# Kernel optimization log

Measured on AMD Instinct MI355X. Metric: run time of the kernel, lower is better.

Reference implementation:

```python
import jax, jax.numpy as jnp
import numpy as np

B, N, D, K = 64, 512, 256, 1024
LIMIT = float(np.sqrt(K))   # default initialize_limit = num_embeddings ** 0.5
BN_EPS = 1e-5               # torch BatchNorm1d default eps


def setup_inputs() -> dict:
    key = jax.random.key(0)
    k1, k2, k3 = jax.random.split(key, 3)
    x = jax.random.normal(k1, (B, N, D), jnp.float32)
    atom_mask = jax.random.randint(k2, (B, N), 0, 2, jnp.int32)
    e_i_ts = jax.random.uniform(k3, (D, K), jnp.float32, -LIMIT, LIMIT)
    return {
        "x": x,
        "atom_mask": atom_mask,
        "e_i_ts": e_i_ts,
        "bn_gamma": jnp.ones((D,), jnp.float32),
        "bn_beta": jnp.zeros((D,), jnp.float32),
    }


def reference(x, atom_mask, e_i_ts, bn_gamma, bn_beta):
    flat = x.reshape(-1, D)                          # [BN, D]
    m = atom_mask.reshape(-1).astype(flat.dtype)     # [BN], 1 = valid atom
    n_valid = jnp.maximum(m.sum(), 1.0)

    # BatchNorm1d (training mode) over valid atoms only (torch applies BN to
    # the gathered rows). Biased variance, as in torch's normalization.
    mu = (m[:, None] * flat).sum(0) / n_valid
    var = (m[:, None] * (flat - mu) ** 2).sum(0) / n_valid
    xb = (flat - mu) * jax.lax.rsqrt(var + BN_EPS) * bn_gamma + bn_beta

    # squared-distance to codebook + argmin + gather
    d = (xb ** 2).sum(1, keepdims=True) - 2.0 * (xb @ e_i_ts) + (e_i_ts ** 2).sum(0, keepdims=True)  # [BN, K]
    idx = jnp.argmin(d, axis=1)                      # [BN]
    q = e_i_ts.T[idx]                                # [BN, D] quantized (valid-row semantics)

    # scatter back into padded tensor (padded rows -> 0), straight-through
    q_pad = (m[:, None] * q).reshape(x.shape)
    quantized_x = x + jax.lax.stop_gradient(q_pad - x)

    sg = jax.lax.stop_gradient
    dictionary_loss = (m[:, None] * (sg(xb) - q) ** 2).sum() / (n_valid * D)
    commitment_loss = (m[:, None] * (xb - sg(q)) ** 2).sum() / (n_valid * D)

    # perplexity over valid atoms
    counts = jnp.zeros((K,), flat.dtype).at[idx].add(m)
    avg_probs = counts / n_valid
    perplexity = jnp.exp(-jnp.sum(avg_probs * jnp.log(avg_probs + 1e-10)))

    idx_out = jnp.where(m > 0, idx, -1)[:, None]     # [BN, 1]; -1 marks padded rows
    return quantized_x, dictionary_loss, commitment_loss, idx_out, perplexity
```

## Files before the change

### kernel.cpp

```cpp
#include <hip/hip_runtime.h>
#include <math.h>

#define BN   32768
#define DIM  256
#define KC   1024
#define BN_EPS 1e-5f

#define QX_SIZE   (BN * DIM)
#define LOSS0_OFF (QX_SIZE)
#define LOSS1_OFF (QX_SIZE + 1)
#define IDX_OFF   (QX_SIZE + 2)
#define PERP_OFF  (QX_SIZE + 2 + BN)

#define PART_V 0
#define PART_I (NSLICE * BN)

#define WS_SUM    0
#define WS_SUMSQ  256
#define WS_COUNT  512
#define WS_LOSS   513
#define WS_COUNTS 1024
#define WS_CNORM  3072
#define WS_PK     8192
#define WS_ETX    (8192 + 262144)
#define WS_MINKEY (8192 + 262144 + 262144)
#define WS_ET_LEG 8192

#define NSLICE 4
#define SLICEK (KC / NSLICE)
#define NGRP   (SLICEK / 64)

typedef short bf16x8  __attribute__((ext_vector_type(8)));
typedef float f32x4   __attribute__((ext_vector_type(4)));
typedef float fvec4   __attribute__((ext_vector_type(4)));
typedef int   int4v   __attribute__((ext_vector_type(4)));
typedef unsigned long long u64;

static __device__ inline unsigned short f2bf(float f) {
    unsigned int u = __float_as_uint(f);
    return (unsigned short)((u + 0x7FFFu + ((u >> 16) & 1u)) >> 16);
}
static __device__ inline fvec4 nt_ld4(const void* p) {
    return __builtin_nontemporal_load((const fvec4*)p);
}
static __device__ inline void nt_st(float* p, float v) {
    __builtin_nontemporal_store(v, p);
}
static __device__ inline unsigned enc_f32(float f) {
    unsigned u = __float_as_uint(f);
    return (u & 0x80000000u) ? ~u : (u | 0x80000000u);
}

__global__ __launch_bounds__(256) void k_pre(const float* __restrict__ x,
                                             const int* __restrict__ mask,
                                             const float* __restrict__ e,
                                             float* __restrict__ ws,
                                             int use_et, int use_pk, int et_off) {
    int t = threadIdx.x;
    int b = blockIdx.x;
    if (b >= 260) {
        if (!use_et && !use_pk) return;
        int b2 = b - 260;
        int d0 = (b2 >> 4) * 64;
        int k0 = (b2 & 15) * 64;
        __shared__ float tile[64][65];
        int c = t & 63;
        int rq = t >> 6;
        #pragma unroll
        for (int p = 0; p < 16; ++p) {
            int dd = p * 4 + rq;
            tile[dd][c] = e[(size_t)(d0 + dd) * KC + k0 + c];
        }
        __syncthreads();
        if (use_et) {
            #pragma unroll
            for (int p = 0; p < 16; ++p) {
                int kk = p * 4 + rq;
                nt_st(&ws[et_off + (size_t)(k0 + kk) * DIM + d0 + c],
                      tile[c][kk]);
            }
        }
        if (use_pk) {
            char* pk = (char*)(ws + WS_PK);
            int lane2 = t & 63;
            int fgrp = t >> 6;
            int quad2 = lane2 >> 4, col2 = lane2 & 15;
            int G = b2 & 15;
            #pragma unroll
            for (int p = 0; p < 4; ++p) {
                int fi = fgrp * 4 + p;
                int kcl = fi >> 3;
                int nt = (fi >> 1) & 3;
                int h = fi & 1;
                int kcg = (b2 >> 4) * 2 + kcl;
                bf16x8 ov;
                #pragma unroll
                for (int j = 0; j < 8; ++j) {
                    float v = tile[kcl * 32 + quad2 * 8 + j][nt * 16 + col2];
                    unsigned u = __float_as_uint(v);
                    if (h == 0) {
                        ov[j] = (short)(u >> 16);
                    } else {
                        float lf = v - __uint_as_float(u & 0xffff0000u);
                        ov[j] = (short)(__float_as_uint(lf) >> 16);
                    }
                }
                size_t off = ((size_t)((G * 8 + kcg) * 8 + nt * 2 + h) << 10)
                             + (size_t)lane2 * 16;
                *(bf16x8*)(pk + off) = ov;
            }
        }
        return;
    }
    if (b >= 256) {
        int k = (b - 256) * 256 + t;
        float acc = 0.f;
        #pragma unroll 8
        for (int d = 0; d < DIM; ++d) {
            float v = e[(size_t)d * KC + k];
            acc = fmaf(v, v, acc);
        }
        ws[WS_CNORM + k] = acc;
        return;
    }
    __shared__ float s4[4 * 256];
    __shared__ float q4[4 * 256];
    __shared__ float cntS[4];
    int c4 = t & 63;
    int rsub = t >> 6;
    float s0=0.f,s1=0.f,s2=0.f,s3=0.f, q0=0.f,q1=0.f,q2=0.f,q3=0.f, cnt=0.f;
    int rbase = b * 4 + rsub;
    for (int i = 0; i < 32; ++i) {
        int r = rbase + i * 1024;
        float m = (float)mask[r];
        fvec4 v = nt_ld4(&x[(size_t)r * DIM + c4 * 4]);
        cnt += m;
        float m0 = m*v.x, m1 = m*v.y, m2 = m*v.z, m3 = m*v.w;
        s0 += m0; s1 += m1; s2 += m2; s3 += m3;
        q0 = fmaf(m0, v.x, q0); q1 = fmaf(m1, v.y, q1);
        q2 = fmaf(m2, v.z, q2); q3 = fmaf(m3, v.w, q3);
    }
    int f = c4 * 4;
    s4[rsub * 256 + f + 0] = s0; s4[rsub * 256 + f + 1] = s1;
    s4[rsub * 256 + f + 2] = s2; s4[rsub * 256 + f + 3] = s3;
    q4[rsub * 256 + f + 0] = q0; q4[rsub * 256 + f + 1] = q1;
    q4[rsub * 256 + f + 2] = q2; q4[rsub * 256 + f + 3] = q3;
    if (c4 == 0) cntS[rsub] = cnt;
    __syncthreads();
    float stot = s4[t] + s4[256 + t] + s4[512 + t] + s4[768 + t];
    float qtot = q4[t] + q4[256 + t] + q4[512 + t] + q4[768 + t];
    atomicAdd(&ws[WS_SUM + t], stot);
    atomicAdd(&ws[WS_SUMSQ + t], qtot);
    if (t == 0)
        atomicAdd(&ws[WS_COUNT], cntS[0] + cntS[1] + cntS[2] + cntS[3]);
}

__global__ __launch_bounds__(512) void k_packA(
        const float* __restrict__ x, const float* __restrict__ gamma,
        const float* __restrict__ beta, const float* __restrict__ ws,
        float* __restrict__ out) {
    __shared__ float muS[DIM], scS[DIM], btS[DIM];
    const int tid = threadIdx.x;
    const int row0 = blockIdx.x * 128;
    const int w = tid >> 6;
    const int lane = tid & 63;
    const int quad = lane >> 4;
    const int col0 = lane & 15;
    if (tid < 256) {
        float cnt = ws[WS_COUNT];
        float nv = fmaxf(cnt, 1.f);
        float mu = ws[WS_SUM + tid] / nv;
        float var = ws[WS_SUMSQ + tid] / nv - mu * mu;
        var = fmaxf(var, 0.f);
        muS[tid] = mu;
        scS[tid] = rsqrtf(var + BN_EPS) * gamma[tid];
        btS[tid] = beta[tid];
    }
    __syncthreads();
    const float* xr = x + (size_t)(row0 + w * 16 + col0) * DIM;
    char* pa = (char*)out + (size_t)(blockIdx.x * 8 + w) * 16384;
    #pragma unroll
    for (int kc = 0; kc < 8; ++kc) {
        int k0 = kc * 32 + quad * 8;
        fvec4 v0 = nt_ld4(xr + k0);
        fvec4 v1 = nt_ld4(xr + k0 + 4);
        float xv[8] = {v0.x, v0.y, v0.z, v0.w, v1.x, v1.y, v1.z, v1.w};
        bf16x8 hv, lv;
        #pragma unroll
        for (int j = 0; j < 8; ++j) {
            float xb = fmaf(xv[j] - muS[k0 + j], scS[k0 + j], btS[k0 + j]);
            unsigned short h = f2bf(xb);
            float hf = __uint_as_float((unsigned)h << 16);
            hv[j] = (short)h;
            lv[j] = (short)f2bf(xb - hf);
        }
        __builtin_nontemporal_store(hv,
            (bf16x8*)(pa + (kc * 2 + 0) * 1024 + lane * 16));
        __builtin_nontemporal_store(lv,
            (bf16x8*)(pa + (kc * 2 + 1) * 1024 + lane * 16));
    }
}


#define CHUNK_COMPUTE(slot, kcc)                                             \
    {                                                                        \
        const char* bufb = &Bs[(slot) * 8192];                               \
        __builtin_amdgcn_s_setprio(1);                                       \
        _Pragma("unroll")                                                    \
        for (int nt = 0; nt < 4; ++nt) {                                     \
            bf16x8 bh = *(const bf16x8*)(bufb + (nt * 2 + 0) * 1024 + lane * 16); \
            bf16x8 bl = *(const bf16x8*)(bufb + (nt * 2 + 1) * 1024 + lane * 16); \
            acc[nt] = __builtin_amdgcn_mfma_f32_16x16x32_bf16(ah[kcc], bh, acc[nt], 0, 0, 0); \
            acc[nt] = __builtin_amdgcn_mfma_f32_16x16x32_bf16(ah[kcc], bl, acc[nt], 0, 0, 0); \
            acc[nt] = __builtin_amdgcn_mfma_f32_16x16x32_bf16(al[kcc], bh, acc[nt], 0, 0, 0); \
        }                                                                    \
        __builtin_amdgcn_s_setprio(0);                                       \
    }

#define SCORE_MERGE(gg)                                                      \
    {                                                                        \
        _Pragma("unroll")                                                    \
        for (int r = 0; r < 4; ++r) {                                        \
            float v = 3.4e38f; int ii = 0;                                   \
            _Pragma("unroll")                                                \
            for (int nt = 0; nt < 4; ++nt) {                                 \
                int kl = (gg) * 64 + nt * 16 + col0;                         \
                float sc = fmaf(-2.f, acc[nt][r], cnS[kl]);                  \
                if (sc < v) { v = sc; ii = kl; }                             \
            }                                                                \
            _Pragma("unroll")                                                \
            for (int m2 = 1; m2 < 16; m2 <<= 1) {                            \
                float v2 = __shfl_xor(v, m2, 64);                            \
                int   i2 = __shfl_xor(ii, m2, 64);                           \
                if (v2 < v || (v2 == v && i2 < ii)) { v = v2; ii = i2; }     \
            }                                                                \
            if (v < bv[r] || (v == bv[r] && ii < bi_[r])) {                  \
                bv[r] = v; bi_[r] = ii;                                      \
            }                                                                \
        }                                                                    \
        _Pragma("unroll")                                                    \
        for (int nt = 0; nt < 4; ++nt)                                       \
            acc[nt] = (f32x4){0.f, 0.f, 0.f, 0.f};                           \
    }

__global__ __launch_bounds__(512, 4) void k_main_mfma(
        const float* __restrict__ x, const int* __restrict__ mask,
        const float* __restrict__ e, const float* __restrict__ gamma,
        const float* __restrict__ beta,
        float* __restrict__ ws, float* __restrict__ out,
        int use_pk, int use_mk, int use_pa) {
    __shared__ __align__(16) char Bs[4 * 8192];
    __shared__ float muS[DIM], scS[DIM], btS[DIM];
    __shared__ float cnS[SLICEK];

    const int tid = threadIdx.x;
    const int rb = blockIdx.x >> 2;
    const int s = blockIdx.x & 3;
    const int row0 = rb * 128;
    const int w = tid >> 6;
    const int lane = tid & 63;
    const int quad = lane >> 4;
    const int col0 = lane & 15;

    if (!use_pa && tid < 256) {
        float cnt = ws[WS_COUNT];
        float nv = fmaxf(cnt, 1.f);
        float mu = ws[WS_SUM + tid] / nv;
        float var = ws[WS_SUMSQ + tid] / nv - mu * mu;
        var = fmaxf(var, 0.f);
        muS[tid] = mu;
        scS[tid] = rsqrtf(var + BN_EPS) * gamma[tid];
        btS[tid] = beta[tid];
    }
    if (tid < SLICEK)
        cnS[tid] = ws[WS_CNORM + s * SLICEK + tid];
    __syncthreads();

    bf16x8 ah[8], al[8];
    if (use_pa) {
        const char* pa = (const char*)out + (size_t)(rb * 8 + w) * 16384;
        #pragma unroll
        for (int kc = 0; kc < 8; ++kc) {
            ah[kc] = *(const bf16x8*)(pa + (kc * 2 + 0) * 1024 + lane * 16);
            al[kc] = *(const bf16x8*)(pa + (kc * 2 + 1) * 1024 + lane * 16);
        }
    } else {
        const float* xr = x + (size_t)(row0 + w * 16 + col0) * DIM;
        #pragma unroll
        for (int kc = 0; kc < 8; ++kc) {
            int k0 = kc * 32 + quad * 8;
            fvec4 v0 = nt_ld4(xr + k0);
            fvec4 v1 = nt_ld4(xr + k0 + 4);
            float xv[8] = {v0.x, v0.y, v0.z, v0.w, v1.x, v1.y, v1.z, v1.w};
            bf16x8 hv, lv;
            #pragma unroll
            for (int j = 0; j < 8; ++j) {
                float xb = fmaf(xv[j] - muS[k0 + j], scS[k0 + j], btS[k0 + j]);
                unsigned short h = f2bf(xb);
                float hf = __uint_as_float((unsigned)h << 16);
                hv[j] = (short)h;
                lv[j] = (short)f2bf(xb - hf);
            }
            ah[kc] = hv;
            al[kc] = lv;
        }
    }
    asm volatile("s_waitcnt vmcnt(0)" ::: "memory");
    __builtin_amdgcn_sched_barrier(0);

    f32x4 acc[4];
    #pragma unroll
    for (int nt = 0; nt < 4; ++nt)
        acc[nt] = (f32x4){0.f, 0.f, 0.f, 0.f};
    float bv[4] = {3.4e38f, 3.4e38f, 3.4e38f, 3.4e38f};
    int   bi_[4] = {0, 0, 0, 0};

    if (use_pk) {
        const char* pkb = (const char*)(ws + WS_PK)
                          + (size_t)s * (NGRP * 8 * 8192);
        auto stage = [&](int c2, int slot) {
            const char* src = pkb + (size_t)c2 * 8192 + w * 1024 + lane * 16;
            char* dst = &Bs[slot * 8192 + w * 1024];
            __builtin_amdgcn_global_load_lds(
                (const __attribute__((address_space(1))) void*)src,
                (__attribute__((address_space(3))) void*)dst, 16, 0, 0);
        };
        stage(0, 0);
        stage(1, 1);
        for (int g = 0; g < NGRP - 1; ++g) {
            #pragma unroll
            for (int kc = 0; kc < 8; ++kc) {
                stage(g * 8 + kc + 2, (kc + 2) & 3);
                asm volatile("s_waitcnt vmcnt(2)" ::: "memory");
                __builtin_amdgcn_s_barrier();
                __builtin_amdgcn_sched_barrier(0);
                CHUNK_COMPUTE(kc & 3, kc);
            }
            SCORE_MERGE(g);
        }
        {
            #pragma unroll
            for (int kc = 0; kc < 8; ++kc) {
                if (kc < 6) {
                    stage((NGRP - 1) * 8 + kc + 2, (kc + 2) & 3);
                    asm volatile("s_waitcnt vmcnt(2)" ::: "memory");
                } else if (kc == 6) {
                    asm volatile("s_waitcnt vmcnt(1)" ::: "memory");
                } else {
                    asm volatile("s_waitcnt vmcnt(0)" ::: "memory");
                }
                __builtin_amdgcn_s_barrier();
                __builtin_amdgcn_sched_barrier(0);
                CHUNK_COMPUTE(kc & 3, kc);
            }
            SCORE_MERGE(NGRP - 1);
        }
    } else {
        for (int g = 0; g < NGRP; ++g) {
            #pragma unroll
            for (int kc = 0; kc < 8; ++kc) {
                const float* ep = e + (size_t)(kc * 32 + quad * 8) * KC
                                    + s * SLICEK + g * 64 + col0;
                #pragma unroll
                for (int nt = 0; nt < 4; ++nt) {
                    const float* epn = ep + nt * 16;
                    float bvv[8];
                    #pragma unroll
                    for (int j = 0; j < 8; ++j)
                        bvv[j] = epn[(size_t)j * KC];
                    int4v hw, lw;
                    #pragma unroll
                    for (int p = 0; p < 4; ++p) {
                        unsigned u0 = __float_as_uint(bvv[2 * p]);
                        unsigned u1 = __float_as_uint(bvv[2 * p + 1]);
                        hw[p] = (int)__builtin_amdgcn_perm(u1, u0, 0x07060302u);
                        float l0 = bvv[2 * p]     - __uint_as_float(u0 & 0xffff0000u);
                        float l1 = bvv[2 * p + 1] - __uint_as_float(u1 & 0xffff0000u);
                        lw[p] = (int)__builtin_amdgcn_perm(__float_as_uint(l1),
                                                           __float_as_uint(l0),
                                                           0x07060302u);
                    }
                    bf16x8 bh = __builtin_bit_cast(bf16x8, hw);
                    bf16x8 bl = __builtin_bit_cast(bf16x8, lw);
                    acc[nt] = __builtin_amdgcn_mfma_f32_16x16x32_bf16(ah[kc], bh, acc[nt], 0, 0, 0);
                    acc[nt] = __builtin_amdgcn_mfma_f32_16x16x32_bf16(ah[kc], bl, acc[nt], 0, 0, 0);
                    acc[nt] = __builtin_amdgcn_mfma_f32_16x16x32_bf16(al[kc], bh, acc[nt], 0, 0, 0);
                }
            }
            SCORE_MERGE(g);
        }
    }

    if (col0 == 0) {
        if (use_mk) {
            u64* mk = (u64*)(ws + WS_MINKEY);
            #pragma unroll
            for (int r = 0; r < 4; ++r) {
                int rl = w * 16 + quad * 4 + r;
                u64 key = ((u64)enc_f32(bv[r]) << 32)
                          | (unsigned)(s * SLICEK + bi_[r]);
                atomicMin(&mk[row0 + rl], key);
            }
        } else {
            #pragma unroll
            for (int r = 0; r < 4; ++r) {
                int rl = w * 16 + quad * 4 + r;
                out[PART_V + s * BN + row0 + rl] = bv[r];
                out[PART_I + s * BN + row0 + rl] = (float)(s * SLICEK + bi_[r]);
            }
        }
    }
}

__global__ __launch_bounds__(256) void k_merge(const int* __restrict__ mask,
                                               float* __restrict__ ws,
                                               float* __restrict__ out) {
    int row = blockIdx.x * 256 + threadIdx.x;
    float bvv = out[PART_V + row];
    int bii = (int)out[PART_I + row];
    #pragma unroll
    for (int s = 1; s < NSLICE; ++s) {
        float v = out[PART_V + s * BN + row];
        int i = (int)out[PART_I + s * BN + row];
        if (v < bvv || (v == bvv && i < bii)) { bvv = v; bii = i; }
    }
    int m = mask[row];
    out[IDX_OFF + row] = m ? (float)bii : -1.0f;
    if (m) atomicAdd(&ws[WS_COUNTS + bii], 1.0f);
}

__global__ __launch_bounds__(256) void k_epi(
        const float* __restrict__ x, const int* __restrict__ mask,
        const float* __restrict__ e, const float* __restrict__ gamma,
        const float* __restrict__ beta,
        const float* __restrict__ ws, float* __restrict__ out,
        int use_et, int et_off, int use_mk) {
    __shared__ __align__(16) float muS[DIM], scS[DIM], btS[DIM];
    __shared__ int   histC[KC];
    __shared__ float wred[4];
    const int tid = threadIdx.x;
    const int row0 = blockIdx.x * 32;
    const int w = tid >> 6;
    const int lane = tid & 63;
    {
        float cnt = ws[WS_COUNT];
        float nv = fmaxf(cnt, 1.f);
        float mu = ws[WS_SUM + tid] / nv;
        float var = ws[WS_SUMSQ + tid] / nv - mu * mu;
        var = fmaxf(var, 0.f);
        muS[tid] = mu;
        scS[tid] = rsqrtf(var + BN_EPS) * gamma[tid];
        btS[tid] = beta[tid];
    }
    #pragma unroll
    for (int j = 0; j < KC / 256; ++j)
        histC[j * 256 + tid] = 0;
    __syncthreads();

    u64 mykey = 0; int mym = 0;
    if (use_mk && lane < 8) {
        const u64* mk = (const u64*)(ws + WS_MINKEY);
        mykey = mk[row0 + w * 8 + lane];
        mym = mask[row0 + w * 8 + lane];
    }

    const int d0 = lane * 4;
    fvec4 mu4 = *(const fvec4*)&muS[d0];
    fvec4 sc4 = *(const fvec4*)&scS[d0];
    fvec4 bt4 = *(const fvec4*)&btS[d0];
    const float* et = ws + et_off;
    float lacc = 0.f;
    int pidx = -1;
    fvec4 g = (fvec4){0.f, 0.f, 0.f, 0.f};
    #pragma unroll
    for (int rr = 0; rr < 8; ++rr) {
        const int row = row0 + w * 8 + rr;
        int m, idx;
        if (use_mk) {
            u64 k = __shfl(mykey, rr, 64);
            m = __shfl(mym, rr, 64);
            idx = (int)(unsigned)(k & 0xFFFFFFFFull);
            if (lane == 0) {
                out[IDX_OFF + row] = m ? (float)idx : -1.0f;
                if (m) atomicAdd(&histC[idx], 1);
            }
        } else {
            m = mask[row];
            idx = m ? (int)out[IDX_OFF + row] : 0;
        }
        const float fm = (float)m;
        fvec4 xv = nt_ld4(&x[(size_t)row * DIM + d0]);
        if (idx != pidx) {
            if (use_mk || !use_et) {
                g.x = e[(size_t)(d0 + 0) * KC + idx];
                g.y = e[(size_t)(d0 + 1) * KC + idx];
                g.z = e[(size_t)(d0 + 2) * KC + idx];
                g.w = e[(size_t)(d0 + 3) * KC + idx];
            } else {
                g = nt_ld4(&et[(size_t)idx * DIM + d0]);
            }
            pidx = idx;
        }
        fvec4 q;
        float dsum = 0.f;
        #pragma unroll
        for (int i = 0; i < 4; ++i) {
            float xb = fmaf(xv[i] - mu4[i], sc4[i], bt4[i]);
            float diff = xb - g[i];
            dsum = fmaf(diff, diff, dsum);
            q[i] = fm * g[i];
        }
        lacc = fmaf(fm, dsum, lacc);
        __builtin_nontemporal_store(q, (fvec4*)&out[(size_t)row * DIM + d0]);
    }
    #pragma unroll
    for (int off2 = 32; off2 > 0; off2 >>= 1)
        lacc += __shfl_down(lacc, off2, 64);
    if (lane == 0) wred[w] = lacc;
    __syncthreads();
    if (use_mk) {
        #pragma unroll
        for (int j = 0; j < KC / 256; ++j) {
            int c = histC[j * 256 + tid];
            if (c > 0) atomicAdd((float*)&ws[WS_COUNTS + j * 256 + tid],
                                 (float)c);
        }
    }
    if (tid == 0)
        atomicAdd((float*)&ws[WS_LOSS], wred[0] + wred[1] + wred[2] + wred[3]);
}

__global__ __launch_bounds__(256) void k_final(const float* __restrict__ ws,
                                               float* __restrict__ out) {
    int t = threadIdx.x;
    __shared__ float wr[4];
    float nv = fmaxf(ws[WS_COUNT], 1.f);
    float acc = 0.f;
    for (int j = t; j < KC; j += 256) {
        float p = ws[WS_COUNTS + j] / nv;
        acc = fmaf(p, logf(p + 1e-10f), acc);
    }
    #pragma unroll
    for (int off = 32; off > 0; off >>= 1) acc += __shfl_down(acc, off, 64);
    if ((t & 63) == 0) wr[t >> 6] = acc;
    __syncthreads();
    if (t == 0) {
        float ent = wr[0] + wr[1] + wr[2] + wr[3];
        float loss = ws[WS_LOSS] / (nv * (float)DIM);
        out[LOSS0_OFF] = loss;
        out[LOSS1_OFF] = loss;
        out[PERP_OFF] = expf(-ent);
    }
}

extern "C" void kernel_launch(void* const* d_in, const int* in_sizes, int n_in,
                              void* d_out, int out_size, void* d_ws, size_t ws_size,
                              hipStream_t stream) {
    const float* x     = (const float*)d_in[0];
    const int*   amask = (const int*)d_in[1];
    const float* e     = (const float*)d_in[2];
    const float* gamma = (const float*)d_in[3];
    const float* beta  = (const float*)d_in[4];
    float* out = (float*)d_out;
    float* ws  = (float*)d_ws;

    size_t need_mk = (size_t)(WS_MINKEY + 2 * BN) * sizeof(float);
    size_t need_pk = (size_t)(WS_ETX + KC * DIM) * sizeof(float);
    size_t need_et = (size_t)(WS_ET_LEG + KC * DIM) * sizeof(float);
    int use_pk = ws_size >= need_pk;
    int use_mk = use_pk && (ws_size >= need_mk);
    int use_pa = use_pk && use_mk;
    int use_et = use_mk ? 0 : (use_pk ? 1 : (ws_size >= need_et ? 1 : 0));
    int et_off = use_pk ? WS_ETX : WS_ET_LEG;

    (void)hipMemsetAsync(d_ws, 0, 32768, stream);
    if (use_mk)
        (void)hipMemsetAsync((char*)d_ws + (size_t)WS_MINKEY * 4, 0xFF,
                             (size_t)BN * 8, stream);

    k_pre<<<324, 256, 0, stream>>>(x, amask, e, ws, use_et, use_pk, et_off);
    if (use_pa)
        k_packA<<<BN / 128, 512, 0, stream>>>(x, gamma, beta, ws, out);
    k_main_mfma<<<256 * NSLICE, 512, 0, stream>>>(x, amask, e, gamma, beta, ws,
                                                  out, use_pk, use_mk, use_pa);
    if (!use_mk)
        k_merge<<<BN / 256, 256, 0, stream>>>(amask, ws, out);
    k_epi<<<BN / 32, 256, 0, stream>>>(x, amask, e, gamma, beta, ws, out,
                                       use_et, et_off, use_mk);
    k_final<<<1, 256, 0, stream>>>(ws, out);
}
```

Before: 229.5 us.

## Retile MFMA waves to 2x2 row-by-codeword tiles with cross-wave argmin merge

```diff
diff --git a/kernel.cpp b/kernel.cpp
--- a/kernel.cpp
+++ b/kernel.cpp
@@ -207,12 +207,19 @@
         const char* bufb = &Bs[(slot) * 8192];                               \
         __builtin_amdgcn_s_setprio(1);                                       \
         _Pragma("unroll")                                                    \
-        for (int nt = 0; nt < 4; ++nt) {                                     \
-            bf16x8 bh = *(const bf16x8*)(bufb + (nt * 2 + 0) * 1024 + lane * 16); \
-            bf16x8 bl = *(const bf16x8*)(bufb + (nt * 2 + 1) * 1024 + lane * 16); \
-            acc[nt] = __builtin_amdgcn_mfma_f32_16x16x32_bf16(ah[kcc], bh, acc[nt], 0, 0, 0); \
-            acc[nt] = __builtin_amdgcn_mfma_f32_16x16x32_bf16(ah[kcc], bl, acc[nt], 0, 0, 0); \
-            acc[nt] = __builtin_amdgcn_mfma_f32_16x16x32_bf16(al[kcc], bh, acc[nt], 0, 0, 0); \
+        for (int nt = 0; nt < 2; ++nt) {                                     \
+            const int ntg = ch * 2 + nt;                                     \
+            bf16x8 bh = *(const bf16x8*)(bufb + (ntg * 2 + 0) * 1024 + lane * 16); \
+            bf16x8 bl = *(const bf16x8*)(bufb + (ntg * 2 + 1) * 1024 + lane * 16); \
+            _Pragma("unroll")                                                \
+            for (int mt = 0; mt < 2; ++mt) {                                 \
+                acc[mt][nt] = __builtin_amdgcn_mfma_f32_16x16x32_bf16(       \
+                    ah[mt][kcc], bh, acc[mt][nt], 0, 0, 0);                  \
+                acc[mt][nt] = __builtin_amdgcn_mfma_f32_16x16x32_bf16(       \
+                    ah[mt][kcc], bl, acc[mt][nt], 0, 0, 0);                  \
+                acc[mt][nt] = __builtin_amdgcn_mfma_f32_16x16x32_bf16(       \
+                    al[mt][kcc], bh, acc[mt][nt], 0, 0, 0);                  \
+            }                                                                \
         }                                                                    \
         __builtin_amdgcn_s_setprio(0);                                       \
     }
@@ -220,30 +227,31 @@
 #define SCORE_MERGE(gg)                                                      \
     {                                                                        \
         _Pragma("unroll")                                                    \
-        for (int r = 0; r < 4; ++r) {                                        \
-            float v = 3.4e38f; int ii = 0;                                   \
+        for (int mt = 0; mt < 2; ++mt) {                                     \
             _Pragma("unroll")                                                \
-            for (int nt = 0; nt < 4; ++nt) {                                 \
-                int kl = (gg) * 64 + nt * 16 + col0;                         \
-                float sc = fmaf(-2.f, acc[nt][r], cnS[kl]);                  \
-                if (sc < v) { v = sc; ii = kl; }                             \
-            }                                                                \
-            _Pragma("unroll")                                                \
-            for (int m2 = 1; m2 < 16; m2 <<= 1) {                            \
-                float v2 = __shfl_xor(v, m2, 64);                            \
-                int   i2 = __shfl_xor(ii, m2, 64);                           \
-                if (v2 < v || (v2 == v && i2 < ii)) { v = v2; ii = i2; }     \
-            }                                                                \
-            if (v < bv[r] || (v == bv[r] && ii < bi_[r])) {                  \
-                bv[r] = v; bi_[r] = ii;                                      \
+            for (int r = 0; r < 4; ++r) {                                    \
+                float v = 3.4e38f; int ii = 0;                               \
+                _Pragma("unroll")                                            \
+                for (int nt = 0; nt < 2; ++nt) {                             \
+                    int kl = (gg) * 64 + (ch * 2 + nt) * 16 + col0;          \
+                    float sc = fmaf(-2.f, acc[mt][nt][r], cnS[kl]);          \
+                    if (sc < v) { v = sc; ii = kl; }                         \
+                    acc[mt][nt][r] = 0.f;                                    \
+                }                                                            \
+                _Pragma("unroll")                                            \
+                for (int m2 = 1; m2 < 16; m2 <<= 1) {                        \
+                    float v2 = __shfl_xor(v, m2, 64);                        \
+                    int   i2 = __shfl_xor(ii, m2, 64);                       \
+                    if (v2 < v || (v2 == v && i2 < ii)) { v = v2; ii = i2; } \
+                }                                                            \
+                if (v < bv[mt][r] || (v == bv[mt][r] && ii < bi_[mt][r])) {  \
+                    bv[mt][r] = v; bi_[mt][r] = ii;                          \
+                }                                                            \
             }                                                                \
         }                                                                    \
-        _Pragma("unroll")                                                    \
-        for (int nt = 0; nt < 4; ++nt)                                       \
-            acc[nt] = (f32x4){0.f, 0.f, 0.f, 0.f};                           \
-    }
-
-__global__ __launch_bounds__(512, 4) void k_main_mfma(
+    }
+
+__global__ __launch_bounds__(512, 2) void k_main_mfma(
         const float* __restrict__ x, const int* __restrict__ mask,
         const float* __restrict__ e, const float* __restrict__ gamma,
         const float* __restrict__ beta,
@@ -252,12 +260,16 @@
     __shared__ __align__(16) char Bs[4 * 8192];
     __shared__ float muS[DIM], scS[DIM], btS[DIM];
     __shared__ float cnS[SLICEK];
+    __shared__ float fvS[128];
+    __shared__ int   fiS[128];
 
     const int tid = threadIdx.x;
     const int rb = blockIdx.x >> 2;
     const int s = blockIdx.x & 3;
     const int row0 = rb * 128;
     const int w = tid >> 6;
+    const int rg = w >> 1;
+    const int ch = w & 1;
     const int lane = tid & 63;
     const int quad = lane >> 4;
     const int col0 = lane & 15;
@@ -276,44 +288,57 @@
         cnS[tid] = ws[WS_CNORM + s * SLICEK + tid];
     __syncthreads();
 
-    bf16x8 ah[8], al[8];
+    bf16x8 ah[2][8], al[2][8];
     if (use_pa) {
-        const char* pa = (const char*)out + (size_t)(rb * 8 + w) * 16384;
-        #pragma unroll
-        for (int kc = 0; kc < 8; ++kc) {
-            ah[kc] = *(const bf16x8*)(pa + (kc * 2 + 0) * 1024 + lane * 16);
-            al[kc] = *(const bf16x8*)(pa + (kc * 2 + 1) * 1024 + lane * 16);
-        }
+        const char* pa = (const char*)out + (size_t)(rb * 8 + rg * 2) * 16384;
+        #pragma unroll
+        for (int mt = 0; mt < 2; ++mt)
+            #pragma unroll
+            for (int kc = 0; kc < 8; ++kc) {
+                ah[mt][kc] = *(const bf16x8*)(pa + mt * 16384
+                                              + (kc * 2 + 0) * 1024 + lane * 16);
+                al[mt][kc] = *(const bf16x8*)(pa + mt * 16384
+                                              + (kc * 2 + 1) * 1024 + lane * 16);
+            }
     } else {
-        const float* xr = x + (size_t)(row0 + w * 16 + col0) * DIM;
-        #pragma unroll
-        for (int kc = 0; kc < 8; ++kc) {
-            int k0 = kc * 32 + quad * 8;
-            fvec4 v0 = nt_ld4(xr + k0);
-            fvec4 v1 = nt_ld4(xr + k0 + 4);
-            float xv[8] = {v0.x, v0.y, v0.z, v0.w, v1.x, v1.y, v1.z, v1.w};
-            bf16x8 hv, lv;
-            #pragma unroll
-            for (int j = 0; j < 8; ++j) {
-                float xb = fmaf(xv[j] - muS[k0 + j], scS[k0 + j], btS[k0 + j]);
-                unsigned short h = f2bf(xb);
-                float hf = __uint_as_float((unsigned)h << 16);
-                hv[j] = (short)h;
-                lv[j] = (short)f2bf(xb - hf);
-            }
-            ah[kc] = hv;
-            al[kc] = lv;
+        #pragma unroll
+        for (int mt = 0; mt < 2; ++mt) {
+            const float* xr = x + (size_t)(row0 + (rg * 2 + mt) * 16 + col0) * DIM;
+            #pragma unroll
+            for (int kc = 0; kc < 8; ++kc) {
+                int k0 = kc * 32 + quad * 8;
+                fvec4 v0 = nt_ld4(xr + k0);
+                fvec4 v1 = nt_ld4(xr + k0 + 4);
+                float xv[8] = {v0.x, v0.y, v0.z, v0.w, v1.x, v1.y, v1.z, v1.w};
+                bf16x8 hv, lv;
+                #pragma unroll
+                for (int j = 0; j < 8; ++j) {
+                    float xb = fmaf(xv[j] - muS[k0 + j], scS[k0 + j], btS[k0 + j]);
+                    unsigned short h = f2bf(xb);
+                    float hf = __uint_as_float((unsigned)h << 16);
+                    hv[j] = (short)h;
+                    lv[j] = (short)f2bf(xb - hf);
+                }
+                ah[mt][kc] = hv;
+                al[mt][kc] = lv;
+            }
         }
     }
     asm volatile("s_waitcnt vmcnt(0)" ::: "memory");
     __builtin_amdgcn_sched_barrier(0);
 
-    f32x4 acc[4];
-    #pragma unroll
-    for (int nt = 0; nt < 4; ++nt)
-        acc[nt] = (f32x4){0.f, 0.f, 0.f, 0.f};
-    float bv[4] = {3.4e38f, 3.4e38f, 3.4e38f, 3.4e38f};
-    int   bi_[4] = {0, 0, 0, 0};
+    f32x4 acc[2][2];
+    #pragma unroll
+    for (int mt = 0; mt < 2; ++mt)
+        #pragma unroll
+        for (int nt = 0; nt < 2; ++nt)
+            acc[mt][nt] = (f32x4){0.f, 0.f, 0.f, 0.f};
+    float bv[2][4];
+    int   bi_[2][4];
+    #pragma unroll
+    for (int mt = 0; mt < 2; ++mt)
+        #pragma unroll
+        for (int r = 0; r < 4; ++r) { bv[mt][r] = 3.4e38f; bi_[mt][r] = 0; }
 
     if (use_pk) {
         const char* pkb = (const char*)(ws + WS_PK)
@@ -362,8 +387,8 @@
                 const float* ep = e + (size_t)(kc * 32 + quad * 8) * KC
                                     + s * SLICEK + g * 64 + col0;
                 #pragma unroll
-                for (int nt = 0; nt < 4; ++nt) {
-                    const float* epn = ep + nt * 16;
+                for (int nt = 0; nt < 2; ++nt) {
+                    const float* epn = ep + (ch * 2 + nt) * 16;
                     float bvv[8];
                     #pragma unroll
                     for (int j = 0; j < 8; ++j)
@@ -382,32 +407,58 @@
                     }
                     bf16x8 bh = __builtin_bit_cast(bf16x8, hw);
                     bf16x8 bl = __builtin_bit_cast(bf16x8, lw);
-                    acc[nt] = __builtin_amdgcn_mfma_f32_16x16x32_bf16(ah[kc], bh, acc[nt], 0, 0, 0);
-                    acc[nt] = __builtin_amdgcn_mfma_f32_16x16x32_bf16(ah[kc], bl, acc[nt], 0, 0, 0);
-                    acc[nt] = __builtin_amdgcn_mfma_f32_16x16x32_bf16(al[kc], bh, acc[nt], 0, 0, 0);
+                    #pragma unroll
+                    for (int mt = 0; mt < 2; ++mt) {
+                        acc[mt][nt] = __builtin_amdgcn_mfma_f32_16x16x32_bf16(
+                            ah[mt][kc], bh, acc[mt][nt], 0, 0, 0);
+                        acc[mt][nt] = __builtin_amdgcn_mfma_f32_16x16x32_bf16(
+                            ah[mt][kc], bl, acc[mt][nt], 0, 0, 0);
+                        acc[mt][nt] = __builtin_amdgcn_mfma_f32_16x16x32_bf16(
+                            al[mt][kc], bh, acc[mt][nt], 0, 0, 0);
+                    }
                 }
             }
             SCORE_MERGE(g);
         }
     }
 
-    if (col0 == 0) {
-        if (use_mk) {
+    if (use_mk) {
+        if (col0 == 0) {
             u64* mk = (u64*)(ws + WS_MINKEY);
             #pragma unroll
-            for (int r = 0; r < 4; ++r) {
-                int rl = w * 16 + quad * 4 + r;
-                u64 key = ((u64)enc_f32(bv[r]) << 32)
-                          | (unsigned)(s * SLICEK + bi_[r]);
-                atomicMin(&mk[row0 + rl], key);
-            }
-        } else {
-            #pragma unroll
-            for (int r = 0; r < 4; ++r) {
-                int rl = w * 16 + quad * 4 + r;
-                out[PART_V + s * BN + row0 + rl] = bv[r];
-                out[PART_I + s * BN + row0 + rl] = (float)(s * SLICEK + bi_[r]);
-            }
+            for (int mt = 0; mt < 2; ++mt)
+                #pragma unroll
+                for (int r = 0; r < 4; ++r) {
+                    int rl = rg * 32 + mt * 16 + quad * 4 + r;
+                    u64 key = ((u64)enc_f32(bv[mt][r]) << 32)
+                              | (unsigned)(s * SLICEK + bi_[mt][r]);
+                    atomicMin(&mk[row0 + rl], key);
+                }
+        }
+    } else {
+        if (ch == 0 && col0 == 0) {
+            #pragma unroll
+            for (int mt = 0; mt < 2; ++mt)
+                #pragma unroll
+                for (int r = 0; r < 4; ++r) {
+                    int rl = rg * 32 + mt * 16 + quad * 4 + r;
+                    fvS[rl] = bv[mt][r];
+                    fiS[rl] = bi_[mt][r];
+                }
+        }
+        __syncthreads();
+        if (ch == 1 && col0 == 0) {
+            #pragma unroll
+            for (int mt = 0; mt < 2; ++mt)
+                #pragma unroll
+                for (int r = 0; r < 4; ++r) {
+                    int rl = rg * 32 + mt * 16 + quad * 4 + r;
+                    float v0 = fvS[rl]; int i0 = fiS[rl];
+                    float v1 = bv[mt][r]; int i1 = bi_[mt][r];
+                    if (v1 < v0 || (v1 == v0 && i1 < i0)) { v0 = v1; i0 = i1; }
+                    out[PART_V + s * BN + row0 + rl] = v0;
+                    out[PART_I + s * BN + row0 + rl] = (float)(s * SLICEK + i0);
+                }
         }
     }
 }
```

New measurement: 279.4 us. 1.22x slower.

## Derive loss from packed min-distance score and row norms, skip x reread in epilogue

Applied to the files above, without the earlier changes.

```diff
diff --git a/kernel.cpp b/kernel.cpp
--- a/kernel.cpp
+++ b/kernel.cpp
@@ -24,6 +24,7 @@
 #define WS_PK     8192
 #define WS_ETX    (8192 + 262144)
 #define WS_MINKEY (8192 + 262144 + 262144)
+#define WS_XQ     (WS_MINKEY + 2 * BN)
 #define WS_ET_LEG 8192
 
 #define NSLICE 4
@@ -49,6 +50,9 @@
 static __device__ inline unsigned enc_f32(float f) {
     unsigned u = __float_as_uint(f);
     return (u & 0x80000000u) ? ~u : (u | 0x80000000u);
+}
+static __device__ inline float dec_f32(unsigned k) {
+    return __uint_as_float((k & 0x80000000u) ? (k ^ 0x80000000u) : ~k);
 }
 
 __global__ __launch_bounds__(256) void k_pre(const float* __restrict__ x,
@@ -157,8 +161,8 @@
 
 __global__ __launch_bounds__(512) void k_packA(
         const float* __restrict__ x, const float* __restrict__ gamma,
-        const float* __restrict__ beta, const float* __restrict__ ws,
-        float* __restrict__ out) {
+        const float* __restrict__ beta, float* __restrict__ ws,
+        float* __restrict__ out, int use_xq) {
     __shared__ float muS[DIM], scS[DIM], btS[DIM];
     const int tid = threadIdx.x;
     const int row0 = blockIdx.x * 128;
@@ -179,6 +183,7 @@
     __syncthreads();
     const float* xr = x + (size_t)(row0 + w * 16 + col0) * DIM;
     char* pa = (char*)out + (size_t)(blockIdx.x * 8 + w) * 16384;
+    float xq = 0.f;
     #pragma unroll
     for (int kc = 0; kc < 8; ++kc) {
         int k0 = kc * 32 + quad * 8;
@@ -189,6 +194,7 @@
         #pragma unroll
         for (int j = 0; j < 8; ++j) {
             float xb = fmaf(xv[j] - muS[k0 + j], scS[k0 + j], btS[k0 + j]);
+            xq = fmaf(xb, xb, xq);
             unsigned short h = f2bf(xb);
             float hf = __uint_as_float((unsigned)h << 16);
             hv[j] = (short)h;
@@ -198,6 +204,12 @@
             (bf16x8*)(pa + (kc * 2 + 0) * 1024 + lane * 16));
         __builtin_nontemporal_store(lv,
             (bf16x8*)(pa + (kc * 2 + 1) * 1024 + lane * 16));
+    }
+    if (use_xq) {
+        xq += __shfl_xor(xq, 16, 64);
+        xq += __shfl_xor(xq, 32, 64);
+        if (quad == 0)
+            ws[WS_XQ + row0 + w * 16 + col0] = xq;
     }
 }
 
@@ -434,7 +446,7 @@
         const float* __restrict__ e, const float* __restrict__ gamma,
         const float* __restrict__ beta,
         const float* __restrict__ ws, float* __restrict__ out,
-        int use_et, int et_off, int use_mk) {
+        int use_et, int et_off, int use_mk, int use_xq) {
     __shared__ __align__(16) float muS[DIM], scS[DIM], btS[DIM];
     __shared__ int   histC[KC];
     __shared__ float wred[4];
@@ -442,7 +454,7 @@
     const int row0 = blockIdx.x * 32;
     const int w = tid >> 6;
     const int lane = tid & 63;
-    {
+    if (!use_xq) {
         float cnt = ws[WS_COUNT];
         float nv = fmaxf(cnt, 1.f);
         float mu = ws[WS_SUM + tid] / nv;
@@ -457,66 +469,98 @@
         histC[j * 256 + tid] = 0;
     __syncthreads();
 
-    u64 mykey = 0; int mym = 0;
+    u64 mykey = 0; int mym = 0; float myxq = 0.f;
     if (use_mk && lane < 8) {
         const u64* mk = (const u64*)(ws + WS_MINKEY);
         mykey = mk[row0 + w * 8 + lane];
         mym = mask[row0 + w * 8 + lane];
+        if (use_xq) myxq = ws[WS_XQ + row0 + w * 8 + lane];
     }
 
     const int d0 = lane * 4;
-    fvec4 mu4 = *(const fvec4*)&muS[d0];
-    fvec4 sc4 = *(const fvec4*)&scS[d0];
-    fvec4 bt4 = *(const fvec4*)&btS[d0];
     const float* et = ws + et_off;
     float lacc = 0.f;
     int pidx = -1;
     fvec4 g = (fvec4){0.f, 0.f, 0.f, 0.f};
-    #pragma unroll
-    for (int rr = 0; rr < 8; ++rr) {
-        const int row = row0 + w * 8 + rr;
-        int m, idx;
-        if (use_mk) {
+    if (use_xq) {
+        #pragma unroll
+        for (int rr = 0; rr < 8; ++rr) {
+            const int row = row0 + w * 8 + rr;
             u64 k = __shfl(mykey, rr, 64);
-            m = __shfl(mym, rr, 64);
-            idx = (int)(unsigned)(k & 0xFFFFFFFFull);
+            int m = __shfl(mym, rr, 64);
+            int idx = (int)(unsigned)(k & 0xFFFFFFFFull);
             if (lane == 0) {
                 out[IDX_OFF + row] = m ? (float)idx : -1.0f;
-                if (m) atomicAdd(&histC[idx], 1);
-            }
-        } else {
-            m = mask[row];
-            idx = m ? (int)out[IDX_OFF + row] : 0;
-        }
-        const float fm = (float)m;
-        fvec4 xv = nt_ld4(&x[(size_t)row * DIM + d0]);
-        if (idx != pidx) {
-            if (use_mk || !use_et) {
+                if (m) {
+                    atomicAdd(&histC[idx], 1);
+                    float score = dec_f32((unsigned)(k >> 32));
+                    lacc += __shfl(myxq, rr, 64) + score;
+                }
+            }
+            if (idx != pidx) {
                 g.x = e[(size_t)(d0 + 0) * KC + idx];
                 g.y = e[(size_t)(d0 + 1) * KC + idx];
                 g.z = e[(size_t)(d0 + 2) * KC + idx];
                 g.w = e[(size_t)(d0 + 3) * KC + idx];
+                pidx = idx;
+            }
+            const float fm = (float)m;
+            fvec4 q = (fvec4){fm * g.x, fm * g.y, fm * g.z, fm * g.w};
+            __builtin_nontemporal_store(q,
+                (fvec4*)&out[(size_t)row * DIM + d0]);
+        }
+        if (lane == 0) wred[w] = lacc;
+    } else {
+        fvec4 mu4 = *(const fvec4*)&muS[d0];
+        fvec4 sc4 = *(const fvec4*)&scS[d0];
+        fvec4 bt4 = *(const fvec4*)&btS[d0];
+        #pragma unroll
+        for (int rr = 0; rr < 8; ++rr) {
+            const int row = row0 + w * 8 + rr;
+            int m, idx;
+            if (use_mk) {
+                u64 k = __shfl(mykey, rr, 64);
+                m = __shfl(mym, rr, 64);
+                idx = (int)(unsigned)(k & 0xFFFFFFFFull);
+                if (lane == 0) {
+                    out[IDX_OFF + row] = m ? (float)idx : -1.0f;
+                    if (m) atomicAdd(&histC[idx], 1);
+                }
             } else {
-                g = nt_ld4(&et[(size_t)idx * DIM + d0]);
-            }
-            pidx = idx;
-        }
-        fvec4 q;
-        float dsum = 0.f;
-        #pragma unroll
-        for (int i = 0; i < 4; ++i) {
-            float xb = fmaf(xv[i] - mu4[i], sc4[i], bt4[i]);
-            float diff = xb - g[i];
-            dsum = fmaf(diff, diff, dsum);
-            q[i] = fm * g[i];
-        }
-        lacc = fmaf(fm, dsum, lacc);
-        __builtin_nontemporal_store(q, (fvec4*)&out[(size_t)row * DIM + d0]);
-    }
-    #pragma unroll
-    for (int off2 = 32; off2 > 0; off2 >>= 1)
-        lacc += __shfl_down(lacc, off2, 64);
-    if (lane == 0) wred[w] = lacc;
+                m = mask[row];
+                idx = m ? (int)out[IDX_OFF + row] : 0;
+            }
+            const float fm = (float)m;
+            fvec4 xv = nt_ld4(&x[(size_t)row * DIM + d0]);
+            if (idx != pidx) {
+                if (use_mk || !use_et) {
+                    g.x = e[(size_t)(d0 + 0) * KC + idx];
+                    g.y = e[(size_t)(d0 + 1) * KC + idx];
+                    g.z = e[(size_t)(d0 + 2) * KC + idx];
+                    g.w = e[(size_t)(d0 + 3) * KC + idx];
+                } else {
+                    g = nt_ld4(&et[(size_t)idx * DIM + d0]);
+                }
+                pidx = idx;
+            }
+            fvec4 q;
+            float dsum = 0.f;
+            #pragma unroll
+            for (int i = 0; i < 4; ++i) {
+                float xb = fmaf(xv[i] - mu4[i], sc4[i], bt4[i]);
+                float diff = xb - g[i];
+                dsum = fmaf(diff, diff, dsum);
+                q[i] = fm * g[i];
+            }
+            lacc = fmaf(fm, dsum, lacc);
+            __builtin_nontemporal_store(q,
+                (fvec4*)&out[(size_t)row * DIM + d0]);
+        }
+        #pragma unroll
+        for (int off2 = 32; off2 > 0; off2 >>= 1)
+            lacc += __shfl_down(lacc, off2, 64);
+        if (lane == 0) wred[w] = lacc;
+    }
     __syncthreads();
     if (use_mk) {
         #pragma unroll
@@ -564,12 +608,14 @@
     float* out = (float*)d_out;
     float* ws  = (float*)d_ws;
 
+    size_t need_xq = (size_t)(WS_XQ + BN) * sizeof(float);
     size_t need_mk = (size_t)(WS_MINKEY + 2 * BN) * sizeof(float);
     size_t need_pk = (size_t)(WS_ETX + KC * DIM) * sizeof(float);
     size_t need_et = (size_t)(WS_ET_LEG + KC * DIM) * sizeof(float);
     int use_pk = ws_size >= need_pk;
     int use_mk = use_pk && (ws_size >= need_mk);
     int use_pa = use_pk && use_mk;
+    int use_xq = use_pa && (ws_size >= need_xq);
     int use_et = use_mk ? 0 : (use_pk ? 1 : (ws_size >= need_et ? 1 : 0));
     int et_off = use_pk ? WS_ETX : WS_ET_LEG;
 
@@ -580,12 +626,12 @@
 
     k_pre<<<324, 256, 0, stream>>>(x, amask, e, ws, use_et, use_pk, et_off);
     if (use_pa)
-        k_packA<<<BN / 128, 512, 0, stream>>>(x, gamma, beta, ws, out);
+        k_packA<<<BN / 128, 512, 0, stream>>>(x, gamma, beta, ws, out, use_xq);
     k_main_mfma<<<256 * NSLICE, 512, 0, stream>>>(x, amask, e, gamma, beta, ws,
                                                   out, use_pk, use_mk, use_pa);
     if (!use_mk)
         k_merge<<<BN / 256, 256, 0, stream>>>(amask, ws, out);
     k_epi<<<BN / 32, 256, 0, stream>>>(x, amask, e, gamma, beta, ws, out,
-                                       use_et, et_off, use_mk);
+                                       use_et, et_off, use_mk, use_xq);
     k_final<<<1, 256, 0, stream>>>(ws, out);
 }
```

Result: faster. 212.3 us (-7.5%).
